# Kernel optimization log

Hardware: AMD Instinct MI355X
Metric: run time of the kernel (lower is better)

The kernel has to match this reference:

```python
import jax, jax.numpy as jnp
import numpy as np
import math

B, C, T, F_IN, F_OUT, H = 4, 8, 512, 512, 512, 8
DK = F_IN // H
NEG_SLOPE = 0.01


def _clinear(xr, xi, Wr, br, Wi, bi):
    # ComplexLinear: (fc_r(xr) - fc_i(xi), fc_r(xi) + fc_i(xr)), each fc has its own bias
    rr = xr @ Wr.T + br
    ii = xi @ Wi.T + bi
    ri = xi @ Wr.T + br
    ir = xr @ Wi.T + bi
    return rr - ii, ri + ir


def _lrelu(x):
    return jnp.where(x >= 0, x, NEG_SLOPE * x)


def setup_inputs() -> dict:
    key = jax.random.key(0)
    ks = jax.random.split(key, 32)
    d = {}
    names = ["query_r", "query_i", "key_r", "key_i", "value_r", "value_i"]
    for n, k in zip(names, ks[:6]):
        d[n] = jax.random.normal(k, (B, C, T, F_IN), dtype=jnp.float32)
    s_in = 1.0 / math.sqrt(F_IN)
    idx = 6
    for p in ["q", "k", "v"]:
        for part in ["r", "i"]:
            d[f"W{p}_{part}"] = jax.random.uniform(ks[idx], (F_IN, F_IN), jnp.float32, -s_in, s_in); idx += 1
            d[f"b{p}_{part}"] = jax.random.uniform(ks[idx], (F_IN,), jnp.float32, -s_in, s_in); idx += 1
    for part in ["r", "i"]:
        d[f"Wo_{part}"] = jax.random.uniform(ks[idx], (F_OUT, F_IN), jnp.float32, -s_in, s_in); idx += 1
        d[f"bo_{part}"] = jax.random.uniform(ks[idx], (F_OUT,), jnp.float32, -s_in, s_in); idx += 1
    return d


def reference(query_r, query_i, key_r, key_i, value_r, value_i,
              Wq_r, bq_r, Wq_i, bq_i, Wk_r, bk_r, Wk_i, bk_i,
              Wv_r, bv_r, Wv_i, bv_i, Wo_r, bo_r, Wo_i, bo_i):
    def split_heads(x):  # (B,C,T,F) -> (B,H,T,C,DK)
        return x.reshape(B, C, T, H, DK).transpose(0, 3, 2, 1, 4)

    qr, qi = _clinear(query_r, query_i, Wq_r, bq_r, Wq_i, bq_i)
    kr, ki = _clinear(key_r, key_i, Wk_r, bk_r, Wk_i, bk_i)
    vr, vi = _clinear(value_r, value_i, Wv_r, bv_r, Wv_i, bv_i)
    qr, qi, kr, ki, vr, vi = map(split_heads, (qr, qi, kr, ki, vr, vi))
    vr, vi = _lrelu(vr), _lrelu(vi)

    # conjugate_transpose_matmul_conjugate: scores over channel dim (B,H,T,C,C)
    qk = lambda a, b: jnp.einsum('bhtcd,bhted->bhtce', a, b)
    scale = 1.0 / math.sqrt(DK)
    sr = (qk(qr, kr) + qk(qi, ki)) * scale
    si = (-qk(qi, kr) + qk(qr, ki)) * scale

    # complex matmul scores @ v (dropout p=0 is identity)
    av = lambda s, v: jnp.einsum('bhtce,bhted->bhtcd', s, v)
    xr = av(sr, vr) - av(si, vi)
    xi = av(si, vr) + av(sr, vi)

    def merge_heads(x):  # (B,H,T,C,DK) -> (B,C,T,H*DK)
        return x.transpose(0, 3, 2, 1, 4).reshape(B, C, T, H * DK)

    xr, xi = _lrelu(merge_heads(xr)), _lrelu(merge_heads(xi))
    return _clinear(xr, xi, Wo_r, bo_r, Wo_i, bo_i)
```

## Files before the change

kernel.cpp:

```cpp
#include <hip/hip_runtime.h>

#define B_  4
#define C_  8
#define T_  512
#define F_  512
#define H_  8
#define M_  (B_*C_*T_)

typedef unsigned short u16;
typedef unsigned int   u32;
typedef __bf16 bf16x8 __attribute__((ext_vector_type(8)));
typedef float  f32x4  __attribute__((ext_vector_type(4)));

__device__ __forceinline__ float bf2f(u16 s) {
    union { u32 u; float f; } c; c.u = ((u32)s) << 16; return c.f;
}
__device__ __forceinline__ u16 f2bf(float f) {
    union { float f; u32 u; } c; c.f = f;
    u32 r = c.u + 0x7fffu + ((c.u >> 16) & 1u);
    return (u16)(r >> 16);
}
__device__ __forceinline__ float bflo(u32 v){ union{u32 u; float f;} c; c.u = v << 16;        return c.f; }
__device__ __forceinline__ float bfhi(u32 v){ union{u32 u; float f;} c; c.u = v & 0xffff0000u; return c.f; }

__device__ __forceinline__ void async16(u16* lds, const u16* g) {
    __builtin_amdgcn_global_load_lds(
        (const __attribute__((address_space(1))) u32*)g,
        (__attribute__((address_space(3))) u32*)lds,
        16, 0, 0);
}

struct ConvArgs { const float* src[6]; u16* dst[6]; };

__global__ __launch_bounds__(256)
void convert6_kernel(ConvArgs a)
{
    const int tid  = threadIdx.x;
    const int base = blockIdx.x * 1024 + tid;
    const float4* s = (const float4*)a.src[blockIdx.y];
    uint4*        d = (uint4*)a.dst[blockIdx.y];

    float4 v[8];
    #pragma unroll
    for (int k = 0; k < 4; ++k) {
        const int o = base + (k << 8);
        v[2*k]     = s[2*o];
        v[2*k + 1] = s[2*o + 1];
    }
    #pragma unroll
    for (int k = 0; k < 4; ++k) {
        const int o = base + (k << 8);
        uint4 u;
        u.x = (u32)f2bf(v[2*k].x)   | ((u32)f2bf(v[2*k].y)   << 16);
        u.y = (u32)f2bf(v[2*k].z)   | ((u32)f2bf(v[2*k].w)   << 16);
        u.z = (u32)f2bf(v[2*k+1].x) | ((u32)f2bf(v[2*k+1].y) << 16);
        u.w = (u32)f2bf(v[2*k+1].z) | ((u32)f2bf(v[2*k+1].w) << 16);
        d[o] = u;
    }
}

struct PrepArgs { const float* wr[4]; const float* wi[4]; const float* br[4]; const float* bi[4]; };

__global__ __launch_bounds__(256)
void prep_weights_kernel(PrepArgs a, u16* __restrict__ wbig, float* __restrict__ bbig)
{
    const int s   = blockIdx.y;
    const int idx = blockIdx.x * 256 + threadIdx.x;
    const int n   = idx >> 8;
    const int k0  = (idx & 255) << 2;
    const int nn = n & 511, kk = k0 & 511;
    const float* src; float sgn = 1.0f;
    if (n < 512) { if (k0 < 512) src = a.wr[s]; else { src = a.wi[s]; sgn = -1.0f; } }
    else         { if (k0 < 512) src = a.wi[s]; else   src = a.wr[s]; }
    const float4 v = *(const float4*)(src + (size_t)nn * 512 + kk);
    ushort4 q;
    q.x = f2bf(sgn * v.x); q.y = f2bf(sgn * v.y);
    q.z = f2bf(sgn * v.z); q.w = f2bf(sgn * v.w);
    *(ushort4*)(wbig + (size_t)s * 1048576 + (size_t)n * 1024 + k0) = q;

    if (blockIdx.x < 4) {
        const int bidx = blockIdx.x * 256 + threadIdx.x;
        const float brv = a.br[s][bidx & 511];
        const float biv = a.bi[s][bidx & 511];
        bbig[s * 1024 + bidx] = (bidx < 512) ? (brv - biv) : (brv + biv);
    }
}

template <bool PERM_OUT, bool LRELU>
__global__ __launch_bounds__(512, 2)
void mfma_clinear256_kernel(const u16* __restrict__ Ar, const u16* __restrict__ Ai,
                            const u16* __restrict__ Wbt, const float* __restrict__ bias,
                            void* __restrict__ Yr_, void* __restrict__ Yi_)
{
    constexpr int SMEM_U16 = PERM_OUT ? (256 * 272) : (256 * 256);
    __shared__ __align__(16) u16 smem[SMEM_U16];
    char* const sm = (char*)smem;

    const int tid  = threadIdx.x;
    const int wv   = tid >> 6;
    const int lane = tid & 63;
    const int m0   = blockIdx.x << 8;
    const int n0   = blockIdx.y << 8;
    const int wm   = (wv >> 2) << 7;
    const int wn   = (wv & 3) << 6;

    const int frow = lane & 15;
    const int fkb  = (lane >> 4) << 4;

    const int srow = tid >> 3;
    const int scol = ((tid & 7) ^ (srow & 7)) << 3;
    const int ldst = wv << 10;

    f32x4 acc[8][4] = {};
    bf16x8 bq[4][2];

    {
        #pragma unroll
        for (int b = 0; b < 4; ++b)
            async16((u16*)(sm + 65536 + b * 8192 + ldst),
                    Wbt + (size_t)(n0 + b * 64 + srow) * 1024 + scol);
        async16((u16*)(sm + 0 * 8192 + ldst), Ar + (size_t)(m0 +   0 + srow) * 512 + scol);
        async16((u16*)(sm + 2 * 8192 + ldst), Ar + (size_t)(m0 + 128 + srow) * 512 + scol);
        async16((u16*)(sm + 1 * 8192 + ldst), Ar + (size_t)(m0 +  64 + srow) * 512 + scol);
        async16((u16*)(sm + 3 * 8192 + ldst), Ar + (size_t)(m0 + 192 + srow) * 512 + scol);
        asm volatile("s_waitcnt vmcnt(2)" ::: "memory");
        asm volatile("s_barrier" ::: "memory");
    }

    for (int tt = 0; tt < 16; ++tt) {
        char* const curA = sm + ((tt & 1) << 15);
        char* const curB = sm + 65536 + ((tt & 1) << 15);
        char* const nxtA = sm + (((tt + 1) & 1) << 15);
        char* const nxtB = sm + 65536 + (((tt + 1) & 1) << 15);
        const bool more = (tt + 1) < 16;
        const u16* An  = ((tt + 1) < 8) ? Ar : Ai;
        const int  akc = ((tt + 1) & 7) << 6;
        const int  bkc = (tt + 1) << 6;

        #pragma unroll
        for (int q = 0; q < 4; ++q) {
            bf16x8 aq[2][2];
            #pragma unroll
            for (int i = 0; i < 2; ++i) {
                const int ra = wm + (2 * q + i) * 16 + frow;
                #pragma unroll
                for (int kk = 0; kk < 2; ++kk) {
                    const int cb = (kk << 6) + fkb;
                    aq[i][kk] = *(const bf16x8*)(curA + ra * 128 + (cb ^ ((ra & 7) << 4)));
                }
            }
            if (q == 0) {
                #pragma unroll
                for (int nf = 0; nf < 4; ++nf) {
                    const int rb = wn + nf * 16 + frow;
                    #pragma unroll
                    for (int kk = 0; kk < 2; ++kk) {
                        const int cb = (kk << 6) + fkb;
                        bq[nf][kk] = *(const bf16x8*)(curB + rb * 128 + (cb ^ ((rb & 7) << 4)));
                    }
                }
            }
            if (more) {
                if (q == 0) {
                    async16((u16*)(nxtB + 0 * 8192 + ldst), Wbt + (size_t)(n0 +   0 + srow) * 1024 + bkc + scol);
                    async16((u16*)(nxtB + 1 * 8192 + ldst), Wbt + (size_t)(n0 +  64 + srow) * 1024 + bkc + scol);
                } else if (q == 1) {
                    async16((u16*)(nxtB + 2 * 8192 + ldst), Wbt + (size_t)(n0 + 128 + srow) * 1024 + bkc + scol);
                    async16((u16*)(nxtB + 3 * 8192 + ldst), Wbt + (size_t)(n0 + 192 + srow) * 1024 + bkc + scol);
                } else if (q == 2) {
                    async16((u16*)(nxtA + 0 * 8192 + ldst), An + (size_t)(m0 +   0 + srow) * 512 + akc + scol);
                    async16((u16*)(nxtA + 2 * 8192 + ldst), An + (size_t)(m0 + 128 + srow) * 512 + akc + scol);
                } else {
                    async16((u16*)(nxtA + 1 * 8192 + ldst), An + (size_t)(m0 +  64 + srow) * 512 + akc + scol);
                    async16((u16*)(nxtA + 3 * 8192 + ldst), An + (size_t)(m0 + 192 + srow) * 512 + akc + scol);
                }
            }
            asm volatile("s_barrier" ::: "memory");
            __builtin_amdgcn_s_setprio(1);
            #pragma unroll
            for (int kk = 0; kk < 2; ++kk)
                #pragma unroll
                for (int i = 0; i < 2; ++i)
                    #pragma unroll
                    for (int nf = 0; nf < 4; ++nf)
                        acc[2 * q + i][nf] = __builtin_amdgcn_mfma_f32_16x16x32_bf16(
                            aq[i][kk], bq[nf][kk], acc[2 * q + i][nf], 0, 0, 0);
            __builtin_amdgcn_s_setprio(0);
            if (q == 1) {
                if (more) asm volatile("s_waitcnt vmcnt(4)" ::: "memory");
                else      asm volatile("s_waitcnt vmcnt(0)" ::: "memory");
            } else if (q == 3) {
                if (more) asm volatile("s_waitcnt vmcnt(2)" ::: "memory");
                else      asm volatile("s_waitcnt vmcnt(0)" ::: "memory");
            }
            asm volatile("s_barrier" ::: "memory");
        }
    }

    const int row_l = (lane >> 4) << 2;

    if constexpr (PERM_OUT) {
        constexpr int LDN = 272;
        #pragma unroll
        for (int mf = 0; mf < 8; ++mf) {
            const int mr = wm + mf * 16 + row_l;
            #pragma unroll
            for (int nf = 0; nf < 4; ++nf) {
                const int ncl = wn + nf * 16 + frow;
                const float bv = bias[n0 + ncl];
                #pragma unroll
                for (int r = 0; r < 4; ++r) {
                    float v = acc[mf][nf][r] + bv;
                    if constexpr (LRELU) v = v >= 0.f ? v : 0.01f * v;
                    smem[(mr + r) * LDN + ncl] = f2bf(v);
                }
            }
        }
        __syncthreads();
        const int part = n0 >> 9;
        u16* Y = part ? (u16*)Yi_ : (u16*)Yr_;
        #pragma unroll
        for (int it = 0; it < 16; ++it) {
            const int idx = (it << 9) + tid;
            const int ml  = idx >> 5;
            const int c8  = (idx & 31) << 3;
            const uint4 dv = *(const uint4*)&smem[ml * LDN + c8];
            const int m  = m0 + ml;
            const int nc = (n0 + c8) & 511;
            const int bb = m >> 12, cc = (m >> 9) & 7, tq = m & 511;
            const int hh = nc >> 6, dd = nc & 63;
            const size_t addr = ((size_t)(((bb << 3) + hh) * T_ + tq) << 9) + (cc << 6) + dd;
            *(uint4*)(Y + addr) = dv;
        }
    } else {
        const int part = n0 >> 9;
        float* Y = part ? (float*)Yi_ : (float*)Yr_;
        #pragma unroll
        for (int nf = 0; nf < 4; ++nf) {
            const int ncol = n0 + wn + nf * 16 + frow;
            const float bv = bias[ncol];
            const int nc = ncol & 511;
            #pragma unroll
            for (int mf = 0; mf < 8; ++mf) {
                const int mb = m0 + wm + mf * 16 + row_l;
                #pragma unroll
                for (int r = 0; r < 4; ++r) {
                    float v = acc[mf][nf][r] + bv;
                    if constexpr (LRELU) v = v >= 0.f ? v : 0.01f * v;
                    Y[(size_t)(mb + r) * 512 + nc] = v;
                }
            }
        }
    }
}

__global__ __launch_bounds__(256)
void attn_kernel(const u16* __restrict__ qr, const u16* __restrict__ qi,
                 const u16* __restrict__ kr, const u16* __restrict__ ki,
                 const u16* __restrict__ vr, const u16* __restrict__ vi,
                 u16* __restrict__ xr, u16* __restrict__ xi)
{
    constexpr int RS = 68;
    constexpr int MS = 8 * RS;
    __shared__ float L[4][6 * MS];
    __shared__ float S[4][128];

    const int wave = threadIdx.x >> 6;
    const int lane = threadIdx.x & 63;
    const int w    = (blockIdx.x << 2) + wave;
    const int cl   = lane >> 3;
    const int dl   = lane & 7;
    const int d0   = dl << 3;

    float* Lw = L[wave];
    const u16* srcs[6] = {qr, qi, kr, ki, vr, vi};
    const size_t gbase = ((size_t)w << 9) + (lane << 3);
    #pragma unroll
    for (int m2 = 0; m2 < 6; ++m2) {
        const uint4 u = *(const uint4*)(srcs[m2] + gbase);
        float* dst = Lw + m2 * MS + cl * RS + d0;
        dst[0]=bflo(u.x); dst[1]=bfhi(u.x);
        dst[2]=bflo(u.y); dst[3]=bfhi(u.y);
        dst[4]=bflo(u.z); dst[5]=bfhi(u.z);
        dst[6]=bflo(u.w); dst[7]=bfhi(u.w);
    }
    __syncthreads();

    {
        const float* Qr = Lw + 0*MS + cl*RS;
        const float* Qi = Lw + 1*MS + cl*RS;
        const float* Kr = Lw + 2*MS + dl*RS;
        const float* Ki = Lw + 3*MS + dl*RS;
        float srr=0.f, sii=0.f, sri=0.f, sir=0.f;
        #pragma unroll 8
        for (int d = 0; d < 64; ++d) {
            srr = fmaf(Qr[d], Kr[d], srr);
            sii = fmaf(Qi[d], Ki[d], sii);
            sri = fmaf(Qr[d], Ki[d], sri);
            sir = fmaf(Qi[d], Kr[d], sir);
        }
        S[wave][lane]      = (srr + sii) * 0.125f;
        S[wave][64 + lane] = (sri - sir) * 0.125f;
    }
    __syncthreads();

    const float* Vr = Lw + 4*MS;
    const float* Vi = Lw + 5*MS;
    const float* Sr = S[wave];
    const float* Si = S[wave] + 64;
    float outr[8] = {}, outi[8] = {};
    #pragma unroll
    for (int e = 0; e < 8; ++e) {
        const float sre = Sr[(cl<<3) + e];
        const float sie = Si[(cl<<3) + e];
        const float* vre = Vr + e*RS + d0;
        const float* vie = Vi + e*RS + d0;
        #pragma unroll
        for (int j = 0; j < 8; ++j) {
            outr[j] = fmaf(sre,  vre[j], outr[j]);
            outr[j] = fmaf(-sie, vie[j], outr[j]);
            outi[j] = fmaf(sie,  vre[j], outi[j]);
            outi[j] = fmaf(sre,  vie[j], outi[j]);
        }
    }

    const int tt = w & 511, hh = (w >> 9) & 7, bb = w >> 12;
    const size_t obase = ((size_t)(((bb << 3) + cl) * T_ + tt) << 9) + (hh << 6) + d0;
    u32 pr[4], pi[4];
    #pragma unroll
    for (int jj = 0; jj < 4; ++jj) {
        float r0 = outr[2*jj], r1 = outr[2*jj+1];
        float i0 = outi[2*jj], i1 = outi[2*jj+1];
        r0 = r0 >= 0.f ? r0 : 0.01f*r0;  r1 = r1 >= 0.f ? r1 : 0.01f*r1;
        i0 = i0 >= 0.f ? i0 : 0.01f*i0;  i1 = i1 >= 0.f ? i1 : 0.01f*i1;
        pr[jj] = (u32)f2bf(r0) | ((u32)f2bf(r1) << 16);
        pi[jj] = (u32)f2bf(i0) | ((u32)f2bf(i1) << 16);
    }
    *(uint4*)(xr + obase) = make_uint4(pr[0], pr[1], pr[2], pr[3]);
    *(uint4*)(xi + obase) = make_uint4(pi[0], pi[1], pi[2], pi[3]);
}

extern "C" void kernel_launch(void* const* d_in, const int* in_sizes, int n_in,
                              void* d_out, int out_size, void* d_ws, size_t ws_size,
                              hipStream_t stream)
{
    (void)in_sizes; (void)n_in; (void)out_size; (void)ws_size;
    const float* act[6];
    for (int i = 0; i < 6; ++i) act[i] = (const float*)d_in[i];

    PrepArgs pa;
    for (int s = 0; s < 4; ++s) {
        pa.wr[s] = (const float*)d_in[6 + s*4 + 0];
        pa.br[s] = (const float*)d_in[6 + s*4 + 1];
        pa.wi[s] = (const float*)d_in[6 + s*4 + 2];
        pa.bi[s] = (const float*)d_in[6 + s*4 + 3];
    }

    const size_t SZ = (size_t)M_ * F_;
    u16* ws = (u16*)d_ws;
    u16* a0 = ws + 0*SZ;  u16* a1 = ws + 1*SZ;
    u16* a2 = ws + 2*SZ;  u16* a3 = ws + 3*SZ;
    u16* a4 = ws + 4*SZ;  u16* a5 = ws + 5*SZ;
    u16* q0 = ws + 6*SZ;  u16* q1 = ws + 7*SZ;
    u16*   wbig = ws + 8*SZ;
    float* bbig = (float*)(wbig + 4u*1024*1024);

    ConvArgs ca;
    ca.src[0]=act[0]; ca.src[1]=act[1]; ca.src[2]=act[2];
    ca.src[3]=act[3]; ca.src[4]=act[4]; ca.src[5]=act[5];
    ca.dst[0]=a0; ca.dst[1]=a1; ca.dst[2]=a2; ca.dst[3]=a3; ca.dst[4]=a4; ca.dst[5]=a5;

    convert6_kernel<<<dim3(1024, 6), 256, 0, stream>>>(ca);
    prep_weights_kernel<<<dim3(1024, 4), 256, 0, stream>>>(pa, wbig, bbig);

    dim3 ggrid(M_/256, 1024/256);
    mfma_clinear256_kernel<true,  false><<<ggrid, 512, 0, stream>>>(
        a0, a1, wbig + 0u*1048576, bbig + 0*1024, q0, q1);
    mfma_clinear256_kernel<true,  false><<<ggrid, 512, 0, stream>>>(
        a2, a3, wbig + 1u*1048576, bbig + 1*1024, a0, a1);
    mfma_clinear256_kernel<true,  true ><<<ggrid, 512, 0, stream>>>(
        a4, a5, wbig + 2u*1048576, bbig + 2*1024, a2, a3);

    attn_kernel<<<dim3((B_*H_*T_)/4), 256, 0, stream>>>(q0, q1, a0, a1, a2, a3, a4, a5);

    float* out_r = (float*)d_out;
    mfma_clinear256_kernel<false, false><<<ggrid, 512, 0, stream>>>(
        a4, a5, wbig + 3u*1048576, bbig + 3*1024, out_r, out_r + SZ);
}
```

Baseline: 441.9 us.

## Fuse fp32-to-bf16 input conversion into projection GEMM loads and remap block order

Removes the separate convert6 kernel. The Q/K/V projection GEMMs now load fp32 activations straight from global memory into registers, convert them to bf16, and write them into swizzled LDS inside the pipelined k-loop. This drops a full write and re-read of six bf16 activation copies. It also remaps the block index so that consecutive blocks share N tiles, for better L2 reuse. The cost is synchronous register-staged A loads with a full vmcnt(0) wait per k-step instead of async global-to-LDS copies, which may reduce load/compute overlap, plus twice the A-tile bytes read from global memory.

```diff
diff --git a/kernel.cpp b/kernel.cpp
--- a/kernel.cpp
+++ b/kernel.cpp
@@ -12,13 +12,15 @@
 typedef __bf16 bf16x8 __attribute__((ext_vector_type(8)));
 typedef float  f32x4  __attribute__((ext_vector_type(4)));
 
-__device__ __forceinline__ float bf2f(u16 s) {
-    union { u32 u; float f; } c; c.u = ((u32)s) << 16; return c.f;
-}
 __device__ __forceinline__ u16 f2bf(float f) {
     union { float f; u32 u; } c; c.f = f;
     u32 r = c.u + 0x7fffu + ((c.u >> 16) & 1u);
     return (u16)(r >> 16);
+}
+__device__ __forceinline__ u32 pk2bf(float a, float b) {
+    union { __bf16 h; u16 u; } x, y;
+    x.h = (__bf16)a; y.h = (__bf16)b;
+    return (u32)x.u | ((u32)y.u << 16);
 }
 __device__ __forceinline__ float bflo(u32 v){ union{u32 u; float f;} c; c.u = v << 16;        return c.f; }
 __device__ __forceinline__ float bfhi(u32 v){ union{u32 u; float f;} c; c.u = v & 0xffff0000u; return c.f; }
@@ -28,35 +30,6 @@
         (const __attribute__((address_space(1))) u32*)g,
         (__attribute__((address_space(3))) u32*)lds,
         16, 0, 0);
-}
-
-struct ConvArgs { const float* src[6]; u16* dst[6]; };
-
-__global__ __launch_bounds__(256)
-void convert6_kernel(ConvArgs a)
-{
-    const int tid  = threadIdx.x;
-    const int base = blockIdx.x * 1024 + tid;
-    const float4* s = (const float4*)a.src[blockIdx.y];
-    uint4*        d = (uint4*)a.dst[blockIdx.y];
-
-    float4 v[8];
-    #pragma unroll
-    for (int k = 0; k < 4; ++k) {
-        const int o = base + (k << 8);
-        v[2*k]     = s[2*o];
-        v[2*k + 1] = s[2*o + 1];
-    }
-    #pragma unroll
-    for (int k = 0; k < 4; ++k) {
-        const int o = base + (k << 8);
-        uint4 u;
-        u.x = (u32)f2bf(v[2*k].x)   | ((u32)f2bf(v[2*k].y)   << 16);
-        u.y = (u32)f2bf(v[2*k].z)   | ((u32)f2bf(v[2*k].w)   << 16);
-        u.z = (u32)f2bf(v[2*k+1].x) | ((u32)f2bf(v[2*k+1].y) << 16);
-        u.w = (u32)f2bf(v[2*k+1].z) | ((u32)f2bf(v[2*k+1].w) << 16);
-        d[o] = u;
-    }
 }
 
 struct PrepArgs { const float* wr[4]; const float* wi[4]; const float* br[4]; const float* bi[4]; };
@@ -86,9 +59,9 @@
     }
 }
 
-template <bool PERM_OUT, bool LRELU>
+template <bool PERM_OUT, bool LRELU, bool A_F32>
 __global__ __launch_bounds__(512, 2)
-void mfma_clinear256_kernel(const u16* __restrict__ Ar, const u16* __restrict__ Ai,
+void mfma_clinear256_kernel(const void* __restrict__ Ar_, const void* __restrict__ Ai_,
                             const u16* __restrict__ Wbt, const float* __restrict__ bias,
                             void* __restrict__ Yr_, void* __restrict__ Yi_)
 {
@@ -99,8 +72,12 @@
     const int tid  = threadIdx.x;
     const int wv   = tid >> 6;
     const int lane = tid & 63;
-    const int m0   = blockIdx.x << 8;
-    const int n0   = blockIdx.y << 8;
+
+    const int id  = blockIdx.y * 64 + blockIdx.x;
+    const int nid = (id & 7) * 32 + (id >> 3);
+    const int m0  = (nid & 63) << 8;
+    const int n0  = (nid >> 6) << 8;
+
     const int wm   = (wv >> 2) << 7;
     const int wn   = (wv & 3) << 6;
 
@@ -108,7 +85,8 @@
     const int fkb  = (lane >> 4) << 4;
 
     const int srow = tid >> 3;
-    const int scol = ((tid & 7) ^ (srow & 7)) << 3;
+    const int sj   = (tid & 7) ^ (srow & 7);
+    const int scol = sj << 3;
     const int ldst = wv << 10;
 
     f32x4 acc[8][4] = {};
@@ -119,11 +97,33 @@
         for (int b = 0; b < 4; ++b)
             async16((u16*)(sm + 65536 + b * 8192 + ldst),
                     Wbt + (size_t)(n0 + b * 64 + srow) * 1024 + scol);
-        async16((u16*)(sm + 0 * 8192 + ldst), Ar + (size_t)(m0 +   0 + srow) * 512 + scol);
-        async16((u16*)(sm + 2 * 8192 + ldst), Ar + (size_t)(m0 + 128 + srow) * 512 + scol);
-        async16((u16*)(sm + 1 * 8192 + ldst), Ar + (size_t)(m0 +  64 + srow) * 512 + scol);
-        async16((u16*)(sm + 3 * 8192 + ldst), Ar + (size_t)(m0 + 192 + srow) * 512 + scol);
-        asm volatile("s_waitcnt vmcnt(2)" ::: "memory");
+        if constexpr (A_F32) {
+            const float* Af = (const float*)Ar_;
+            float4 av[8];
+            #pragma unroll
+            for (int b = 0; b < 4; ++b) {
+                const float* src = Af + (size_t)(m0 + b * 64 + srow) * 512 + scol;
+                av[2*b]   = *(const float4*)(src);
+                av[2*b+1] = *(const float4*)(src + 4);
+            }
+            #pragma unroll
+            for (int b = 0; b < 4; ++b) {
+                uint4 w;
+                w.x = pk2bf(av[2*b].x,   av[2*b].y);
+                w.y = pk2bf(av[2*b].z,   av[2*b].w);
+                w.z = pk2bf(av[2*b+1].x, av[2*b+1].y);
+                w.w = pk2bf(av[2*b+1].z, av[2*b+1].w);
+                *(uint4*)(sm + b * 8192 + (srow << 7) + ((tid & 7) << 4)) = w;
+            }
+            asm volatile("s_waitcnt vmcnt(0) lgkmcnt(0)" ::: "memory");
+        } else {
+            const u16* Ab = (const u16*)Ar_;
+            async16((u16*)(sm + 0 * 8192 + ldst), Ab + (size_t)(m0 +   0 + srow) * 512 + scol);
+            async16((u16*)(sm + 2 * 8192 + ldst), Ab + (size_t)(m0 + 128 + srow) * 512 + scol);
+            async16((u16*)(sm + 1 * 8192 + ldst), Ab + (size_t)(m0 +  64 + srow) * 512 + scol);
+            async16((u16*)(sm + 3 * 8192 + ldst), Ab + (size_t)(m0 + 192 + srow) * 512 + scol);
+            asm volatile("s_waitcnt vmcnt(2)" ::: "memory");
+        }
         asm volatile("s_barrier" ::: "memory");
     }
 
@@ -133,9 +133,10 @@
         char* const nxtA = sm + (((tt + 1) & 1) << 15);
         char* const nxtB = sm + 65536 + (((tt + 1) & 1) << 15);
         const bool more = (tt + 1) < 16;
-        const u16* An  = ((tt + 1) < 8) ? Ar : Ai;
         const int  akc = ((tt + 1) & 7) << 6;
         const int  bkc = (tt + 1) << 6;
+
+        float4 av[8];
 
         #pragma unroll
         for (int q = 0; q < 4; ++q) {
@@ -160,19 +161,50 @@
                     }
                 }
             }
-            if (more) {
-                if (q == 0) {
-                    async16((u16*)(nxtB + 0 * 8192 + ldst), Wbt + (size_t)(n0 +   0 + srow) * 1024 + bkc + scol);
-                    async16((u16*)(nxtB + 1 * 8192 + ldst), Wbt + (size_t)(n0 +  64 + srow) * 1024 + bkc + scol);
-                } else if (q == 1) {
-                    async16((u16*)(nxtB + 2 * 8192 + ldst), Wbt + (size_t)(n0 + 128 + srow) * 1024 + bkc + scol);
-                    async16((u16*)(nxtB + 3 * 8192 + ldst), Wbt + (size_t)(n0 + 192 + srow) * 1024 + bkc + scol);
-                } else if (q == 2) {
-                    async16((u16*)(nxtA + 0 * 8192 + ldst), An + (size_t)(m0 +   0 + srow) * 512 + akc + scol);
-                    async16((u16*)(nxtA + 2 * 8192 + ldst), An + (size_t)(m0 + 128 + srow) * 512 + akc + scol);
-                } else {
-                    async16((u16*)(nxtA + 1 * 8192 + ldst), An + (size_t)(m0 +  64 + srow) * 512 + akc + scol);
-                    async16((u16*)(nxtA + 3 * 8192 + ldst), An + (size_t)(m0 + 192 + srow) * 512 + akc + scol);
+            if constexpr (A_F32) {
+                if (more) {
+                    if (q == 0) {
+                        const float* Af = (const float*)(((tt + 1) < 8) ? Ar_ : Ai_);
+                        #pragma unroll
+                        for (int b = 0; b < 4; ++b) {
+                            const float* src = Af + (size_t)(m0 + b * 64 + srow) * 512 + akc + scol;
+                            av[2*b]   = *(const float4*)(src);
+                            av[2*b+1] = *(const float4*)(src + 4);
+                        }
+                        async16((u16*)(nxtB + 0 * 8192 + ldst), Wbt + (size_t)(n0 +   0 + srow) * 1024 + bkc + scol);
+                        async16((u16*)(nxtB + 1 * 8192 + ldst), Wbt + (size_t)(n0 +  64 + srow) * 1024 + bkc + scol);
+                    } else if (q == 1) {
+                        async16((u16*)(nxtB + 2 * 8192 + ldst), Wbt + (size_t)(n0 + 128 + srow) * 1024 + bkc + scol);
+                        async16((u16*)(nxtB + 3 * 8192 + ldst), Wbt + (size_t)(n0 + 192 + srow) * 1024 + bkc + scol);
+                    } else if (q == 2) {
+                        #pragma unroll
+                        for (int b = 0; b < 4; ++b) {
+                            uint4 w;
+                            w.x = pk2bf(av[2*b].x,   av[2*b].y);
+                            w.y = pk2bf(av[2*b].z,   av[2*b].w);
+                            w.z = pk2bf(av[2*b+1].x, av[2*b+1].y);
+                            w.w = pk2bf(av[2*b+1].z, av[2*b+1].w);
+                            *(uint4*)(nxtA + b * 8192 + (srow << 7) + ((tid & 7) << 4)) = w;
+                        }
+                        asm volatile("s_waitcnt lgkmcnt(0)" ::: "memory");
+                    }
+                }
+            } else {
+                const u16* An = (const u16*)(((tt + 1) < 8) ? Ar_ : Ai_);
+                if (more) {
+                    if (q == 0) {
+                        async16((u16*)(nxtB + 0 * 8192 + ldst), Wbt + (size_t)(n0 +   0 + srow) * 1024 + bkc + scol);
+                        async16((u16*)(nxtB + 1 * 8192 + ldst), Wbt + (size_t)(n0 +  64 + srow) * 1024 + bkc + scol);
+                    } else if (q == 1) {
+                        async16((u16*)(nxtB + 2 * 8192 + ldst), Wbt + (size_t)(n0 + 128 + srow) * 1024 + bkc + scol);
+                        async16((u16*)(nxtB + 3 * 8192 + ldst), Wbt + (size_t)(n0 + 192 + srow) * 1024 + bkc + scol);
+                    } else if (q == 2) {
+                        async16((u16*)(nxtA + 0 * 8192 + ldst), An + (size_t)(m0 +   0 + srow) * 512 + akc + scol);
+                        async16((u16*)(nxtA + 2 * 8192 + ldst), An + (size_t)(m0 + 128 + srow) * 512 + akc + scol);
+                    } else {
+                        async16((u16*)(nxtA + 1 * 8192 + ldst), An + (size_t)(m0 +  64 + srow) * 512 + akc + scol);
+                        async16((u16*)(nxtA + 3 * 8192 + ldst), An + (size_t)(m0 + 192 + srow) * 512 + akc + scol);
+                    }
                 }
             }
             asm volatile("s_barrier" ::: "memory");
@@ -186,12 +218,17 @@
                         acc[2 * q + i][nf] = __builtin_amdgcn_mfma_f32_16x16x32_bf16(
                             aq[i][kk], bq[nf][kk], acc[2 * q + i][nf], 0, 0, 0);
             __builtin_amdgcn_s_setprio(0);
-            if (q == 1) {
-                if (more) asm volatile("s_waitcnt vmcnt(4)" ::: "memory");
-                else      asm volatile("s_waitcnt vmcnt(0)" ::: "memory");
-            } else if (q == 3) {
-                if (more) asm volatile("s_waitcnt vmcnt(2)" ::: "memory");
-                else      asm volatile("s_waitcnt vmcnt(0)" ::: "memory");
+            if constexpr (A_F32) {
+                if (q == 3)
+                    asm volatile("s_waitcnt vmcnt(0)" ::: "memory");
+            } else {
+                if (q == 1) {
+                    if (more) asm volatile("s_waitcnt vmcnt(4)" ::: "memory");
+                    else      asm volatile("s_waitcnt vmcnt(0)" ::: "memory");
+                } else if (q == 3) {
+                    if (more) asm volatile("s_waitcnt vmcnt(2)" ::: "memory");
+                    else      asm volatile("s_waitcnt vmcnt(0)" ::: "memory");
+                }
             }
             asm volatile("s_barrier" ::: "memory");
         }
@@ -365,25 +402,19 @@
     u16*   wbig = ws + 8*SZ;
     float* bbig = (float*)(wbig + 4u*1024*1024);
 
-    ConvArgs ca;
-    ca.src[0]=act[0]; ca.src[1]=act[1]; ca.src[2]=act[2];
-    ca.src[3]=act[3]; ca.src[4]=act[4]; ca.src[5]=act[5];
-    ca.dst[0]=a0; ca.dst[1]=a1; ca.dst[2]=a2; ca.dst[3]=a3; ca.dst[4]=a4; ca.dst[5]=a5;
-
-    convert6_kernel<<<dim3(1024, 6), 256, 0, stream>>>(ca);
     prep_weights_kernel<<<dim3(1024, 4), 256, 0, stream>>>(pa, wbig, bbig);
 
     dim3 ggrid(M_/256, 1024/256);
-    mfma_clinear256_kernel<true,  false><<<ggrid, 512, 0, stream>>>(
-        a0, a1, wbig + 0u*1048576, bbig + 0*1024, q0, q1);
-    mfma_clinear256_kernel<true,  false><<<ggrid, 512, 0, stream>>>(
-        a2, a3, wbig + 1u*1048576, bbig + 1*1024, a0, a1);
-    mfma_clinear256_kernel<true,  true ><<<ggrid, 512, 0, stream>>>(
-        a4, a5, wbig + 2u*1048576, bbig + 2*1024, a2, a3);
+    mfma_clinear256_kernel<true,  false, true><<<ggrid, 512, 0, stream>>>(
+        act[0], act[1], wbig + 0u*1048576, bbig + 0*1024, q0, q1);
+    mfma_clinear256_kernel<true,  false, true><<<ggrid, 512, 0, stream>>>(
+        act[2], act[3], wbig + 1u*1048576, bbig + 1*1024, a0, a1);
+    mfma_clinear256_kernel<true,  true,  true><<<ggrid, 512, 0, stream>>>(
+        act[4], act[5], wbig + 2u*1048576, bbig + 2*1024, a2, a3);
 
     attn_kernel<<<dim3((B_*H_*T_)/4), 256, 0, stream>>>(q0, q1, a0, a1, a2, a3, a4, a5);
 
     float* out_r = (float*)d_out;
-    mfma_clinear256_kernel<false, false><<<ggrid, 512, 0, stream>>>(
+    mfma_clinear256_kernel<false, false, false><<<ggrid, 512, 0, stream>>>(
         a4, a5, wbig + 3u*1048576, bbig + 3*1024, out_r, out_r + SZ);
 }
```

Result: slower. 483.0 us (+9.3%).

## Deepen GEMM prefetch pipeline, swap grid order, and pad epilogue LDS stride

Applied to the files above, without the earlier changes.

Restructures the complex-linear GEMM main loop so that global-to-LDS loads are issued up to two k-tiles ahead, with a uniform vmcnt(6) wait and a peeled final iteration. It also swaps the grid axes so consecutive blocks cover the N dimension of the same M rows, which should improve L2 reuse of the activation tile. The epilogue LDS row stride changes from 272 to 280 to reduce bank conflicts. The deeper prefetch keeps more loads in flight but relies on careful buffer-reuse ordering and adds an lgkmcnt wait before each MFMA group.

```diff
diff --git a/kernel.cpp b/kernel.cpp
--- a/kernel.cpp
+++ b/kernel.cpp
@@ -12,9 +12,6 @@
 typedef __bf16 bf16x8 __attribute__((ext_vector_type(8)));
 typedef float  f32x4  __attribute__((ext_vector_type(4)));
 
-__device__ __forceinline__ float bf2f(u16 s) {
-    union { u32 u; float f; } c; c.u = ((u32)s) << 16; return c.f;
-}
 __device__ __forceinline__ u16 f2bf(float f) {
     union { float f; u32 u; } c; c.f = f;
     u32 r = c.u + 0x7fffu + ((c.u >> 16) & 1u);
@@ -92,15 +89,18 @@
                             const u16* __restrict__ Wbt, const float* __restrict__ bias,
                             void* __restrict__ Yr_, void* __restrict__ Yi_)
 {
-    constexpr int SMEM_U16 = PERM_OUT ? (256 * 272) : (256 * 256);
+    constexpr int LDN = 280;
+    constexpr int SMEM_U16 = PERM_OUT ? (256 * LDN) : (256 * 256);
     __shared__ __align__(16) u16 smem[SMEM_U16];
     char* const sm = (char*)smem;
 
     const int tid  = threadIdx.x;
     const int wv   = tid >> 6;
     const int lane = tid & 63;
-    const int m0   = blockIdx.x << 8;
-    const int n0   = blockIdx.y << 8;
+
+    const int m0  = blockIdx.y << 8;
+    const int n0  = blockIdx.x << 8;
+
     const int wm   = (wv >> 2) << 7;
     const int wn   = (wv & 3) << 6;
 
@@ -111,32 +111,30 @@
     const int scol = ((tid & 7) ^ (srow & 7)) << 3;
     const int ldst = wv << 10;
 
+    auto stageA = [&](int tl, int qa) {
+        const u16* An = (tl < 8) ? Ar : Ai;
+        async16((u16*)(sm + ((tl & 1) << 15) + qa * 8192 + ldst),
+                An + (size_t)(m0 + qa * 64 + srow) * 512 + ((tl & 7) << 6) + scol);
+    };
+    auto stageB = [&](int tl, int c) {
+        async16((u16*)(sm + 65536 + ((tl & 1) << 15) + c * 8192 + ldst),
+                Wbt + (size_t)(n0 + c * 64 + srow) * 1024 + (tl << 6) + scol);
+    };
+
     f32x4 acc[8][4] = {};
     bf16x8 bq[4][2];
 
-    {
-        #pragma unroll
-        for (int b = 0; b < 4; ++b)
-            async16((u16*)(sm + 65536 + b * 8192 + ldst),
-                    Wbt + (size_t)(n0 + b * 64 + srow) * 1024 + scol);
-        async16((u16*)(sm + 0 * 8192 + ldst), Ar + (size_t)(m0 +   0 + srow) * 512 + scol);
-        async16((u16*)(sm + 2 * 8192 + ldst), Ar + (size_t)(m0 + 128 + srow) * 512 + scol);
-        async16((u16*)(sm + 1 * 8192 + ldst), Ar + (size_t)(m0 +  64 + srow) * 512 + scol);
-        async16((u16*)(sm + 3 * 8192 + ldst), Ar + (size_t)(m0 + 192 + srow) * 512 + scol);
-        asm volatile("s_waitcnt vmcnt(2)" ::: "memory");
-        asm volatile("s_barrier" ::: "memory");
-    }
-
-    for (int tt = 0; tt < 16; ++tt) {
-        char* const curA = sm + ((tt & 1) << 15);
-        char* const curB = sm + 65536 + ((tt & 1) << 15);
-        char* const nxtA = sm + (((tt + 1) & 1) << 15);
-        char* const nxtB = sm + 65536 + (((tt + 1) & 1) << 15);
-        const bool more = (tt + 1) < 16;
-        const u16* An  = ((tt + 1) < 8) ? Ar : Ai;
-        const int  akc = ((tt + 1) & 7) << 6;
-        const int  bkc = (tt + 1) << 6;
-
+    stageA(0, 0); stageA(0, 2);
+    stageB(0, 0); stageB(0, 1); stageB(0, 2); stageB(0, 3);
+    stageA(0, 1); stageA(0, 3);
+    stageA(1, 0); stageA(1, 2);
+    stageB(1, 0); stageB(1, 1);
+    asm volatile("s_waitcnt vmcnt(4)" ::: "memory");
+    asm volatile("s_barrier" ::: "memory");
+
+    for (int t = 0; t < 15; ++t) {
+        char* const curA = sm + ((t & 1) << 15);
+        char* const curB = sm + 65536 + ((t & 1) << 15);
         #pragma unroll
         for (int q = 0; q < 4; ++q) {
             bf16x8 aq[2][2];
@@ -146,7 +144,8 @@
                 #pragma unroll
                 for (int kk = 0; kk < 2; ++kk) {
                     const int cb = (kk << 6) + fkb;
-                    aq[i][kk] = *(const bf16x8*)(curA + ra * 128 + (cb ^ ((ra & 7) << 4)));
+                    aq[i][kk] = *(const bf16x8*)(curA + (ra >> 6) * 8192 + (ra & 63) * 128
+                                                 + (cb ^ ((ra & 7) << 4)));
                 }
             }
             if (q == 0) {
@@ -156,26 +155,18 @@
                     #pragma unroll
                     for (int kk = 0; kk < 2; ++kk) {
                         const int cb = (kk << 6) + fkb;
-                        bq[nf][kk] = *(const bf16x8*)(curB + rb * 128 + (cb ^ ((rb & 7) << 4)));
+                        bq[nf][kk] = *(const bf16x8*)(curB + (rb >> 6) * 8192 + (rb & 63) * 128
+                                                      + (cb ^ ((rb & 7) << 4)));
                     }
                 }
             }
-            if (more) {
-                if (q == 0) {
-                    async16((u16*)(nxtB + 0 * 8192 + ldst), Wbt + (size_t)(n0 +   0 + srow) * 1024 + bkc + scol);
-                    async16((u16*)(nxtB + 1 * 8192 + ldst), Wbt + (size_t)(n0 +  64 + srow) * 1024 + bkc + scol);
-                } else if (q == 1) {
-                    async16((u16*)(nxtB + 2 * 8192 + ldst), Wbt + (size_t)(n0 + 128 + srow) * 1024 + bkc + scol);
-                    async16((u16*)(nxtB + 3 * 8192 + ldst), Wbt + (size_t)(n0 + 192 + srow) * 1024 + bkc + scol);
-                } else if (q == 2) {
-                    async16((u16*)(nxtA + 0 * 8192 + ldst), An + (size_t)(m0 +   0 + srow) * 512 + akc + scol);
-                    async16((u16*)(nxtA + 2 * 8192 + ldst), An + (size_t)(m0 + 128 + srow) * 512 + akc + scol);
-                } else {
-                    async16((u16*)(nxtA + 1 * 8192 + ldst), An + (size_t)(m0 +  64 + srow) * 512 + akc + scol);
-                    async16((u16*)(nxtA + 3 * 8192 + ldst), An + (size_t)(m0 + 192 + srow) * 512 + akc + scol);
-                }
-            }
+            if (q == 0)      { stageB(t + 1, 2); stageB(t + 1, 3); }
+            else if (q == 1) { stageA(t + 1, 1); stageA(t + 1, 3); }
+            else if (q == 2) { if (t + 2 < 16) { stageA(t + 2, 0); stageA(t + 2, 2); } }
+            else             { if (t + 2 < 16) { stageB(t + 2, 0); stageB(t + 2, 1); } }
+
             asm volatile("s_barrier" ::: "memory");
+            asm volatile("s_waitcnt lgkmcnt(0)" ::: "memory");
             __builtin_amdgcn_s_setprio(1);
             #pragma unroll
             for (int kk = 0; kk < 2; ++kk)
@@ -186,21 +177,57 @@
                         acc[2 * q + i][nf] = __builtin_amdgcn_mfma_f32_16x16x32_bf16(
                             aq[i][kk], bq[nf][kk], acc[2 * q + i][nf], 0, 0, 0);
             __builtin_amdgcn_s_setprio(0);
-            if (q == 1) {
-                if (more) asm volatile("s_waitcnt vmcnt(4)" ::: "memory");
-                else      asm volatile("s_waitcnt vmcnt(0)" ::: "memory");
-            } else if (q == 3) {
-                if (more) asm volatile("s_waitcnt vmcnt(2)" ::: "memory");
-                else      asm volatile("s_waitcnt vmcnt(0)" ::: "memory");
-            }
+            if (t == 14 && q == 3) asm volatile("s_waitcnt vmcnt(0)" ::: "memory");
+            else                   asm volatile("s_waitcnt vmcnt(6)" ::: "memory");
             asm volatile("s_barrier" ::: "memory");
         }
     }
 
+    {
+        char* const curA = sm + (1 << 15);
+        char* const curB = sm + 65536 + (1 << 15);
+        #pragma unroll
+        for (int q = 0; q < 4; ++q) {
+            bf16x8 aq[2][2];
+            #pragma unroll
+            for (int i = 0; i < 2; ++i) {
+                const int ra = wm + (2 * q + i) * 16 + frow;
+                #pragma unroll
+                for (int kk = 0; kk < 2; ++kk) {
+                    const int cb = (kk << 6) + fkb;
+                    aq[i][kk] = *(const bf16x8*)(curA + (ra >> 6) * 8192 + (ra & 63) * 128
+                                                 + (cb ^ ((ra & 7) << 4)));
+                }
+            }
+            if (q == 0) {
+                #pragma unroll
+                for (int nf = 0; nf < 4; ++nf) {
+                    const int rb = wn + nf * 16 + frow;
+                    #pragma unroll
+                    for (int kk = 0; kk < 2; ++kk) {
+                        const int cb = (kk << 6) + fkb;
+                        bq[nf][kk] = *(const bf16x8*)(curB + (rb >> 6) * 8192 + (rb & 63) * 128
+                                                      + (cb ^ ((rb & 7) << 4)));
+                    }
+                }
+            }
+            __builtin_amdgcn_s_setprio(1);
+            #pragma unroll
+            for (int kk = 0; kk < 2; ++kk)
+                #pragma unroll
+                for (int i = 0; i < 2; ++i)
+                    #pragma unroll
+                    for (int nf = 0; nf < 4; ++nf)
+                        acc[2 * q + i][nf] = __builtin_amdgcn_mfma_f32_16x16x32_bf16(
+                            aq[i][kk], bq[nf][kk], acc[2 * q + i][nf], 0, 0, 0);
+            __builtin_amdgcn_s_setprio(0);
+        }
+    }
+    __syncthreads();
+
     const int row_l = (lane >> 4) << 2;
 
     if constexpr (PERM_OUT) {
-        constexpr int LDN = 272;
         #pragma unroll
         for (int mf = 0; mf < 8; ++mf) {
             const int mr = wm + mf * 16 + row_l;
@@ -373,7 +400,7 @@
     convert6_kernel<<<dim3(1024, 6), 256, 0, stream>>>(ca);
     prep_weights_kernel<<<dim3(1024, 4), 256, 0, stream>>>(pa, wbig, bbig);
 
-    dim3 ggrid(M_/256, 1024/256);
+    dim3 ggrid(1024/256, M_/256);
     mfma_clinear256_kernel<true,  false><<<ggrid, 512, 0, stream>>>(
         a0, a1, wbig + 0u*1048576, bbig + 0*1024, q0, q1);
     mfma_clinear256_kernel<true,  false><<<ggrid, 512, 0, stream>>>(
```

After: 446.6 us. No clear change (+1.1%).
